# Kernel optimization log

Measured on AMD Instinct MI355X. Metric: run time of the kernel, lower is better.

## Reference

```python
import jax, jax.numpy as jnp
import numpy as np

B, S, H, NH, I = 8, 1024, 1024, 16, 4096
HD = H // NH
EPS = 1e-6
NEG = -1e9


def _glorot(key, shape):
    lim = np.sqrt(6.0 / (shape[0] + shape[1]))
    return jax.random.uniform(key, shape, jnp.float32, -lim, lim)


def setup_inputs() -> dict:
    key = jax.random.key(0)
    ks = jax.random.split(key, 8)
    return {
        "inputs": jax.random.normal(ks[0], (B, S, H), jnp.float32),
        "inputs_mask": jnp.zeros((B, S), jnp.float32),  # 1.0 marks padding
        "attn_qkvw": _glorot(ks[1], (H, 3 * H)),
        "attn_qkvb": jnp.zeros((3 * H,), jnp.float32),
        "attn_ow": _glorot(ks[2], (H, H)),
        "attn_ob": jnp.zeros((H,), jnp.float32),
        "attn_nw": jnp.ones((H,), jnp.float32),
        "attn_nb": jnp.zeros((H,), jnp.float32),
        "inter_w": _glorot(ks[3], (H, I)),
        "inter_b": jnp.zeros((I,), jnp.float32),
        "output_w": _glorot(ks[4], (I, H)),
        "output_b": jnp.zeros((H,), jnp.float32),
        "ffn_nw": jnp.ones((H,), jnp.float32),
        "ffn_nb": jnp.zeros((H,), jnp.float32),
    }


def _layer_norm(x, g, b):
    m = jnp.mean(x, axis=-1, keepdims=True)
    v = jnp.mean(jnp.square(x - m), axis=-1, keepdims=True)
    return (x - m) * jax.lax.rsqrt(v + EPS) * g + b


def reference(inputs, inputs_mask, attn_qkvw, attn_qkvb, attn_ow, attn_ob,
              attn_nw, attn_nb, inter_w, inter_b, output_w, output_b,
              ffn_nw, ffn_nb):
    # ---- self-attention block (pre-LN) ----
    res = inputs
    x = _layer_norm(inputs, attn_nw, attn_nb)
    qkv = x @ attn_qkvw + attn_qkvb                      # [B,S,3H]
    q, k, v = jnp.split(qkv, 3, axis=-1)
    q = q.reshape(B, S, NH, HD)
    k = k.reshape(B, S, NH, HD)
    v = v.reshape(B, S, NH, HD)
    scale = 1.0 / np.sqrt(HD)
    scores = jnp.einsum("bqhd,bkhd->bhqk", q, k) * scale
    scores = scores + inputs_mask[:, None, None, :] * NEG
    probs = jax.nn.softmax(scores, axis=-1)
    ctx = jnp.einsum("bhqk,bkhd->bqhd", probs, v).reshape(B, S, H)
    attn_out = ctx @ attn_ow + attn_ob
    x = res + attn_out
    # ---- FFN block (pre-LN, ReLU) ----
    res2 = x
    y = _layer_norm(x, ffn_nw, ffn_nb)
    h = jax.nn.relu(y @ inter_w + inter_b)
    return res2 + h @ output_w + output_b
```

## Files before the change

### kernel.cpp

```cpp
#include <hip/hip_runtime.h>
#include <cstdint>
#include <cstddef>

typedef _Float16 f16;
typedef _Float16 half8 __attribute__((ext_vector_type(8)));
typedef _Float16 half4v __attribute__((ext_vector_type(4)));
typedef float floatx4 __attribute__((ext_vector_type(4)));
typedef float floatx16 __attribute__((ext_vector_type(16)));

__device__ __forceinline__ floatx4 mfma16(half8 a, half8 b, floatx4 c) {
    return __builtin_amdgcn_mfma_f32_16x16x32_f16(a, b, c, 0, 0, 0);
}
__device__ __forceinline__ floatx16 mfma32(half8 a, half8 b, floatx16 c) {
    return __builtin_amdgcn_mfma_f32_32x32x16_f16(a, b, c, 0, 0, 0);
}

__device__ __forceinline__ void async16(const f16* g, f16* l) {
    __builtin_amdgcn_global_load_lds(
        (const __attribute__((address_space(1))) unsigned int*)(uintptr_t)g,
        (__attribute__((address_space(3))) unsigned int*)(uintptr_t)l,
        16, 0, 0);
}

__global__ __launch_bounds__(256)
void ln_f16_kernel(const float* __restrict__ x, const float* __restrict__ g,
                   const float* __restrict__ be, f16* __restrict__ y)
{
    int row = blockIdx.x, t = threadIdx.x;
    const float* xr = x + (size_t)row * 1024;
    float4 v = *(const float4*)(xr + t * 4);
    float s1 = v.x + v.y + v.z + v.w;
    float s2 = v.x * v.x + v.y * v.y + v.z * v.z + v.w * v.w;
    #pragma unroll
    for (int off = 32; off >= 1; off >>= 1) {
        s1 += __shfl_xor(s1, off);
        s2 += __shfl_xor(s2, off);
    }
    __shared__ float r1[4], r2[4];
    if ((t & 63) == 0) { r1[t >> 6] = s1; r2[t >> 6] = s2; }
    __syncthreads();
    s1 = r1[0] + r1[1] + r1[2] + r1[3];
    s2 = r2[0] + r2[1] + r2[2] + r2[3];
    float mean = s1 * 0.0009765625f;
    float var  = s2 * 0.0009765625f - mean * mean;
    float rs = rsqrtf(var + 1e-6f);
    float4 gv = *(const float4*)(g + t * 4);
    float4 bv = *(const float4*)(be + t * 4);
    half4v o;
    o[0] = (f16)((v.x - mean) * rs * gv.x + bv.x);
    o[1] = (f16)((v.y - mean) * rs * gv.y + bv.y);
    o[2] = (f16)((v.z - mean) * rs * gv.z + bv.z);
    o[3] = (f16)((v.w - mean) * rs * gv.w + bv.w);
    *(half4v*)(y + (size_t)row * 1024 + t * 4) = o;
}

__global__ __launch_bounds__(256)
void transpose_f16_kernel(const float* __restrict__ W, f16* __restrict__ WT,
                          int R, int C)
{
    __shared__ float tile[32][33];
    int tx = threadIdx.x & 31, ty0 = threadIdx.x >> 5;
    int r0 = blockIdx.y * 32, c0 = blockIdx.x * 32;
    #pragma unroll
    for (int i = 0; i < 4; ++i)
        tile[ty0 + i * 8][tx] = W[(size_t)(r0 + ty0 + i * 8) * C + c0 + tx];
    __syncthreads();
    #pragma unroll
    for (int i = 0; i < 4; ++i)
        WT[(size_t)(c0 + ty0 + i * 8) * R + r0 + tx] = (f16)tile[tx][ty0 + i * 8];
}

__global__ __launch_bounds__(256, 2)
void gemm_kernel(const f16* __restrict__ A, const f16* __restrict__ BT,
                 const float* __restrict__ bias, const float* __restrict__ res,
                 float* __restrict__ Cf32, int M, int N, int K)
{
    __shared__ __align__(16) f16 As[2][128 * 64];
    __shared__ __align__(16) f16 Bs[2][128 * 64];
    int m0 = blockIdx.x * 128, n0 = blockIdx.y * 128;
    int t = threadIdx.x, lane = t & 63, wave = t >> 6;
    int quad = lane >> 4, l16 = lane & 15;
    int wm = (wave & 1) * 64, wn = (wave >> 1) * 64;
    int sw = l16 & 7;
    floatx4 acc[4][4] = {};

    const f16* gA[4]; const f16* gB[4]; int oS[4];
    #pragma unroll
    for (int c = 0; c < 4; ++c) {
        int s = c * 256 + t;
        int row = s >> 3, lg = (s & 7) ^ (row & 7);
        gA[c] = A  + (size_t)(m0 + row) * K + lg * 8;
        gB[c] = BT + (size_t)(n0 + row) * K + lg * 8;
        oS[c] = (c * 256 + (t & ~63)) * 8;
    }

    #pragma unroll
    for (int c = 0; c < 4; ++c) {
        async16(gA[c], As[0] + oS[c]);
        async16(gB[c], Bs[0] + oS[c]);
    }
    __syncthreads();

    int buf = 0;
    for (int k0 = 0; k0 < K; k0 += 64) {
        int kn = k0 + 64;
        if (kn < K) {
            #pragma unroll
            for (int c = 0; c < 4; ++c) {
                async16(gA[c] + kn, As[buf ^ 1] + oS[c]);
                async16(gB[c] + kn, Bs[buf ^ 1] + oS[c]);
            }
        }
        #pragma unroll
        for (int ks = 0; ks < 2; ++ks) {
            int ca = (ks * 4 + quad) ^ sw;
            half8 a[4], b[4];
            #pragma unroll
            for (int i = 0; i < 4; ++i) {
                a[i] = *(const half8*)(As[buf] + (wm + i * 16 + l16) * 64 + ca * 8);
                b[i] = *(const half8*)(Bs[buf] + (wn + i * 16 + l16) * 64 + ca * 8);
            }
            #pragma unroll
            for (int i = 0; i < 4; ++i)
                #pragma unroll
                for (int j = 0; j < 4; ++j)
                    acc[i][j] = mfma16(a[i], b[j], acc[i][j]);
        }
        __syncthreads();
        buf ^= 1;
    }

    #pragma unroll
    for (int j = 0; j < 4; ++j) {
        int col = n0 + wn + j * 16 + l16;
        float bv = bias[col];
        #pragma unroll
        for (int i = 0; i < 4; ++i) {
            int rowb = m0 + wm + i * 16 + quad * 4;
            #pragma unroll
            for (int r = 0; r < 4; ++r) {
                float v = acc[i][j][r] + bv;
                size_t idx = (size_t)(rowb + r) * N + col;
                Cf32[idx] = v + res[idx];
            }
        }
    }
}

template<int MODE>
__global__ __launch_bounds__(256, 2)
void gemm_big_kernel(const f16* __restrict__ A, const f16* __restrict__ BT,
                     const float* __restrict__ bias, f16* __restrict__ Cf16,
                     f16* __restrict__ qb, f16* __restrict__ kb, f16* __restrict__ vb,
                     int M, int N, int K)
{
    __shared__ __align__(16) f16 As[2][256 * 32];
    __shared__ __align__(16) f16 Bs[2][128 * 32];
    int m0 = blockIdx.x * 256, n0 = blockIdx.y * 128;
    int t = threadIdx.x, lane = t & 63, wave = t >> 6;
    int l32 = lane & 31, kg = lane >> 5;
    int swz = (l32 ^ (l32 >> 2) ^ (l32 >> 4)) & 3;
    floatx16 acc[2][4];
    #pragma unroll
    for (int mi = 0; mi < 2; ++mi)
        #pragma unroll
        for (int jn = 0; jn < 4; ++jn)
            #pragma unroll
            for (int r = 0; r < 16; ++r) acc[mi][jn][r] = 0.f;

    const f16* gA[4]; int oA[4];
    #pragma unroll
    for (int c = 0; c < 4; ++c) {
        int s = c * 256 + t;
        int row = s >> 2, phys = s & 3;
        int lg = phys ^ ((row ^ (row >> 2) ^ (row >> 4)) & 3);
        gA[c] = A + (size_t)(m0 + row) * K + lg * 8;
        oA[c] = (c * 256 + (t & ~63)) * 8;
    }
    const f16* gB[2]; int oB[2];
    #pragma unroll
    for (int c = 0; c < 2; ++c) {
        int s = c * 256 + t;
        int row = s >> 2, phys = s & 3;
        int lg = phys ^ ((row ^ (row >> 2) ^ (row >> 4)) & 3);
        gB[c] = BT + (size_t)(n0 + row) * K + lg * 8;
        oB[c] = (c * 256 + (t & ~63)) * 8;
    }

    #pragma unroll
    for (int c = 0; c < 4; ++c) async16(gA[c], As[0] + oA[c]);
    #pragma unroll
    for (int c = 0; c < 2; ++c) async16(gB[c], Bs[0] + oB[c]);
    __syncthreads();

    int buf = 0;
    for (int k0 = 0; k0 < K; k0 += 32) {
        int kn = k0 + 32;
        if (kn < K) {
            #pragma unroll
            for (int c = 0; c < 4; ++c) async16(gA[c] + kn, As[buf ^ 1] + oA[c]);
            #pragma unroll
            for (int c = 0; c < 2; ++c) async16(gB[c] + kn, Bs[buf ^ 1] + oB[c]);
        }
        #pragma unroll
        for (int ss = 0; ss < 2; ++ss) {
            int cb = ss * 2 + kg;
            half8 a[2], b[4];
            #pragma unroll
            for (int mi = 0; mi < 2; ++mi) {
                int ca = (cb ^ swz ^ (mi * 2));
                a[mi] = *(const half8*)(As[buf] + (wave * 64 + mi * 32 + l32) * 32 + ca * 8);
            }
            #pragma unroll
            for (int jn = 0; jn < 4; ++jn) {
                int ca = (cb ^ swz ^ ((jn & 1) * 2));
                b[jn] = *(const half8*)(Bs[buf] + (jn * 32 + l32) * 32 + ca * 8);
            }
            #pragma unroll
            for (int mi = 0; mi < 2; ++mi)
                #pragma unroll
                for (int jn = 0; jn < 4; ++jn)
                    acc[mi][jn] = mfma32(a[mi], b[jn], acc[mi][jn]);
        }
        __syncthreads();
        buf ^= 1;
    }

    #pragma unroll
    for (int mi = 0; mi < 2; ++mi) {
        int mbase = m0 + wave * 64 + mi * 32 + 4 * kg;
        #pragma unroll
        for (int jn = 0; jn < 4; ++jn) {
            int col = n0 + jn * 32 + l32;
            float bv = bias[col];
            if (MODE == 1) {
                #pragma unroll
                for (int reg = 0; reg < 16; ++reg) {
                    int row = mbase + (reg & 3) + 8 * (reg >> 2);
                    Cf16[(size_t)row * N + col] = (f16)fmaxf(acc[mi][jn][reg] + bv, 0.f);
                }
            } else {
                int part = col >> 10;
                int h = (col >> 6) & 15;
                int d = col & 63;
                if (part == 2) {
                    #pragma unroll
                    for (int rb = 0; rb < 4; ++rb) {
                        int m = mbase + 8 * rb;
                        int bb = m >> 10, s = m & 1023;
                        size_t bh = (size_t)bb * 16 + h;
                        half4v pv;
                        #pragma unroll
                        for (int r = 0; r < 4; ++r) pv[r] = (f16)(acc[mi][jn][rb * 4 + r] + bv);
                        *(half4v*)(vb + (bh * 64 + d) * 1024 + s) = pv;
                    }
                } else {
                    f16* dst0 = part == 0 ? qb : kb;
                    #pragma unroll
                    for (int reg = 0; reg < 16; ++reg) {
                        int m = mbase + (reg & 3) + 8 * (reg >> 2);
                        int bb = m >> 10, s = m & 1023;
                        size_t bh = (size_t)bb * 16 + h;
                        dst0[(bh * 1024 + s) * 64 + d] = (f16)(acc[mi][jn][reg] + bv);
                    }
                }
            }
        }
    }
}

__global__ __launch_bounds__(256)
void attn_kernel(const f16* __restrict__ qb, const f16* __restrict__ kb,
                 const f16* __restrict__ vb, const float* __restrict__ mask,
                 f16* __restrict__ ctx)
{
    const int S = 1024;
    int qt = blockIdx.x, h = blockIdx.y, b = blockIdx.z;
    size_t bh = (size_t)b * 16 + h;
    int t = threadIdx.x, lane = t & 63, wv = t >> 6;
    int quad = lane >> 4, l16 = lane & 15;
    int sw = l16 & 7;

    __shared__ __align__(16) f16 Ks[64 * 64];
    __shared__ __align__(16) f16 Vs[64 * 64];
    __shared__ __align__(16) f16 Ps[4][16 * 40];

    int q0 = qt * 64 + wv * 16;
    const f16* qrow = qb + (bh * 1024 + q0 + l16) * 64;
    half8 aq0 = *(const half8*)(qrow + quad * 8);
    half8 aq1 = *(const half8*)(qrow + 32 + quad * 8);

    floatx4 o[4] = {};
    float lsum[4] = {0.f, 0.f, 0.f, 0.f};
    const float scale = 0.125f;
    const float* mrow = mask + b * S;

    for (int kc = 0; kc < S; kc += 64) {
        __syncthreads();
        #pragma unroll
        for (int c = 0; c < 2; ++c) {
            int s = c * 256 + t;
            int row = s >> 3, phys = s & 7;
            int lg = phys ^ (row & 7);
            f16* lk = Ks + (size_t)(c * 256 + (t & ~63)) * 8;
            f16* lv = Vs + (size_t)(c * 256 + (t & ~63)) * 8;
            async16(kb + (bh * 1024 + kc + row) * 64 + lg * 8, lk);
            async16(vb + (bh * 64 + row) * 1024 + kc + lg * 8, lv);
        }
        __syncthreads();

        floatx4 sf[4];
        #pragma unroll
        for (int cg = 0; cg < 4; ++cg) {
            const f16* kr = Ks + (cg * 16 + l16) * 64;
            int c0 = quad ^ sw;
            half8 b0 = *(const half8*)(kr + c0 * 8);
            half8 b1 = *(const half8*)(kr + (c0 ^ 4) * 8);
            floatx4 z = {};
            sf[cg] = mfma16(aq1, b1, mfma16(aq0, b0, z));
        }
        #pragma unroll
        for (int cg = 0; cg < 4; ++cg) {
            float mk = mrow[kc + cg * 16 + l16] * (-1e9f);
            #pragma unroll
            for (int r = 0; r < 4; ++r) {
                float e = __expf(sf[cg][r] * scale + mk);
                lsum[r] += e;
                Ps[wv][(quad * 4 + r) * 40 + cg * 16 + l16] = (f16)e;
            }
        }
        half8 ap0 = *(const half8*)(Ps[wv] + l16 * 40 + quad * 8);
        half8 ap1 = *(const half8*)(Ps[wv] + l16 * 40 + 32 + quad * 8);
        #pragma unroll
        for (int td = 0; td < 4; ++td) {
            const f16* vr = Vs + (td * 16 + l16) * 64;
            int c0 = quad ^ sw;
            half8 bv0 = *(const half8*)(vr + c0 * 8);
            half8 bv1 = *(const half8*)(vr + (c0 ^ 4) * 8);
            o[td] = mfma16(ap0, bv0, o[td]);
            o[td] = mfma16(ap1, bv1, o[td]);
        }
    }

    #pragma unroll
    for (int r = 0; r < 4; ++r) {
        float s = lsum[r];
        s += __shfl_xor(s, 1); s += __shfl_xor(s, 2);
        s += __shfl_xor(s, 4); s += __shfl_xor(s, 8);
        lsum[r] = 1.f / s;
    }
    #pragma unroll
    for (int td = 0; td < 4; ++td)
        #pragma unroll
        for (int r = 0; r < 4; ++r)
            ctx[((size_t)b * 1024 + q0 + quad * 4 + r) * 1024 + h * 64 + td * 16 + l16]
                = (f16)(o[td][r] * lsum[r]);
}

extern "C" void kernel_launch(void* const* d_in, const int* in_sizes, int n_in,
                              void* d_out, int out_size, void* d_ws, size_t ws_size,
                              hipStream_t stream)
{
    const float* inputs = (const float*)d_in[0];
    const float* mask   = (const float*)d_in[1];
    const float* qkvw   = (const float*)d_in[2];
    const float* qkvb   = (const float*)d_in[3];
    const float* ow     = (const float*)d_in[4];
    const float* ob     = (const float*)d_in[5];
    const float* anw    = (const float*)d_in[6];
    const float* anb    = (const float*)d_in[7];
    const float* iw     = (const float*)d_in[8];
    const float* ib     = (const float*)d_in[9];
    const float* outw   = (const float*)d_in[10];
    const float* outb   = (const float*)d_in[11];
    const float* fnw    = (const float*)d_in[12];
    const float* fnb    = (const float*)d_in[13];
    float* out = (float*)d_out;

    const int M = 8192;
    uint8_t* ws = (uint8_t*)d_ws;
    f16* wT_qkv = (f16*)(ws + 0);
    f16* wT_o   = (f16*)(ws + 6291456);
    f16* wT_i   = (f16*)(ws + 8388608);
    f16* wT_out = (f16*)(ws + 16777216);
    f16* xln    = (f16*)(ws + 25165824);
    float* x1   = (float*)(ws + 41943040);
    f16* qbuf   = (f16*)(ws + 75497472);
    f16* kbuf   = (f16*)(ws + 92274688);
    f16* vbuf   = (f16*)(ws + 109051904);
    f16* ctx    = (f16*)(ws + 125829120);
    f16* hbuf   = (f16*)(ws + 75497472);

    transpose_f16_kernel<<<dim3(96, 32),  256, 0, stream>>>(qkvw, wT_qkv, 1024, 3072);
    transpose_f16_kernel<<<dim3(32, 32),  256, 0, stream>>>(ow,   wT_o,   1024, 1024);
    transpose_f16_kernel<<<dim3(128, 32), 256, 0, stream>>>(iw,   wT_i,   1024, 4096);
    transpose_f16_kernel<<<dim3(32, 128), 256, 0, stream>>>(outw, wT_out, 4096, 1024);

    ln_f16_kernel<<<8192, 256, 0, stream>>>(inputs, anw, anb, xln);

    gemm_big_kernel<2><<<dim3(32, 24), 256, 0, stream>>>(xln, wT_qkv, qkvb,
        nullptr, qbuf, kbuf, vbuf, M, 3072, 1024);

    attn_kernel<<<dim3(16, 16, 8), 256, 0, stream>>>(qbuf, kbuf, vbuf, mask, ctx);

    gemm_kernel<<<dim3(64, 8), 256, 0, stream>>>(ctx, wT_o, ob, inputs,
        x1, M, 1024, 1024);

    ln_f16_kernel<<<8192, 256, 0, stream>>>(x1, fnw, fnb, xln);

    gemm_big_kernel<1><<<dim3(32, 32), 256, 0, stream>>>(xln, wT_i, ib,
        hbuf, nullptr, nullptr, nullptr, M, 4096, 1024);

    gemm_kernel<<<dim3(64, 8), 256, 0, stream>>>(hbuf, wT_out, outb, x1,
        out, M, 1024, 4096);
}
```

Before: 494.9 us.

## Triple-buffer big GEMM LDS staging with partial vmcnt waits and MFMA priority

Moves the big GEMM kernel from double to triple buffering of the A/B LDS tiles, prefetching two k-steps ahead. It replaces the full __syncthreads drain with s_waitcnt vmcnt(6) plus s_barrier, so one stage of async loads can stay in flight across the barrier. The MFMA block is wrapped in s_setprio to favour matrix issue. LDS use rises from 48KB to 72KB per block, which may hurt the 2-blocks-per-CU occupancy target.

```diff
diff --git a/kernel.cpp b/kernel.cpp
--- a/kernel.cpp
+++ b/kernel.cpp
@@ -147,6 +147,13 @@
     }
 }
 
+#define BSTAGE(bi, kk) do {                                                    \
+    _Pragma("unroll")                                                          \
+    for (int c = 0; c < 4; ++c) async16(gA[c] + (kk), As[bi] + oA[c]);         \
+    _Pragma("unroll")                                                          \
+    for (int c = 0; c < 2; ++c) async16(gB[c] + (kk), Bs[bi] + oB[c]);         \
+} while (0)
+
 template<int MODE>
 __global__ __launch_bounds__(256, 2)
 void gemm_big_kernel(const f16* __restrict__ A, const f16* __restrict__ BT,
@@ -154,8 +161,8 @@
                      f16* __restrict__ qb, f16* __restrict__ kb, f16* __restrict__ vb,
                      int M, int N, int K)
 {
-    __shared__ __align__(16) f16 As[2][256 * 32];
-    __shared__ __align__(16) f16 Bs[2][128 * 32];
+    __shared__ __align__(16) f16 As[3][256 * 32];
+    __shared__ __align__(16) f16 Bs[3][128 * 32];
     int m0 = blockIdx.x * 256, n0 = blockIdx.y * 128;
     int t = threadIdx.x, lane = t & 63, wave = t >> 6;
     int l32 = lane & 31, kg = lane >> 5;
@@ -187,21 +194,17 @@
         oB[c] = (c * 256 + (t & ~63)) * 8;
     }
 
-    #pragma unroll
-    for (int c = 0; c < 4; ++c) async16(gA[c], As[0] + oA[c]);
-    #pragma unroll
-    for (int c = 0; c < 2; ++c) async16(gB[c], Bs[0] + oB[c]);
-    __syncthreads();
-
-    int buf = 0;
+    BSTAGE(0, 0);
+    BSTAGE(1, 32);
+    asm volatile("s_waitcnt vmcnt(6)" ::: "memory");
+    __builtin_amdgcn_s_barrier();
+
+    int bi = 0;
+    #pragma unroll 1
     for (int k0 = 0; k0 < K; k0 += 32) {
-        int kn = k0 + 32;
-        if (kn < K) {
-            #pragma unroll
-            for (int c = 0; c < 4; ++c) async16(gA[c] + kn, As[buf ^ 1] + oA[c]);
-            #pragma unroll
-            for (int c = 0; c < 2; ++c) async16(gB[c] + kn, Bs[buf ^ 1] + oB[c]);
-        }
+        int kn = k0 + 64;
+        int bs = bi + 2; if (bs >= 3) bs -= 3;
+        if (kn < K) BSTAGE(bs, kn);
         #pragma unroll
         for (int ss = 0; ss < 2; ++ss) {
             int cb = ss * 2 + kg;
@@ -209,21 +212,25 @@
             #pragma unroll
             for (int mi = 0; mi < 2; ++mi) {
                 int ca = (cb ^ swz ^ (mi * 2));
-                a[mi] = *(const half8*)(As[buf] + (wave * 64 + mi * 32 + l32) * 32 + ca * 8);
+                a[mi] = *(const half8*)(As[bi] + (wave * 64 + mi * 32 + l32) * 32 + ca * 8);
             }
             #pragma unroll
             for (int jn = 0; jn < 4; ++jn) {
                 int ca = (cb ^ swz ^ ((jn & 1) * 2));
-                b[jn] = *(const half8*)(Bs[buf] + (jn * 32 + l32) * 32 + ca * 8);
-            }
+                b[jn] = *(const half8*)(Bs[bi] + (jn * 32 + l32) * 32 + ca * 8);
+            }
+            __builtin_amdgcn_s_setprio(1);
             #pragma unroll
             for (int mi = 0; mi < 2; ++mi)
                 #pragma unroll
                 for (int jn = 0; jn < 4; ++jn)
                     acc[mi][jn] = mfma32(a[mi], b[jn], acc[mi][jn]);
-        }
-        __syncthreads();
-        buf ^= 1;
+            __builtin_amdgcn_s_setprio(0);
+        }
+        if (kn < K) { asm volatile("s_waitcnt vmcnt(6)" ::: "memory"); }
+        else        { asm volatile("s_waitcnt vmcnt(0)" ::: "memory"); }
+        __builtin_amdgcn_s_barrier();
+        bi = bi + 1; if (bi >= 3) bi = 0;
     }
 
     #pragma unroll
@@ -268,6 +275,7 @@
         }
     }
 }
+#undef BSTAGE
 
 __global__ __launch_bounds__(256)
 void attn_kernel(const f16* __restrict__ qb, const f16* __restrict__ kb,
```

Result: faster. 478.3 us (-3.4%).

## Double-buffer K/V tiles in attention kernel to overlap loads with compute

Applied to the files above, without the earlier changes.

Adds a second LDS buffer for the K and V tiles and issues the async global-to-LDS loads for the next 64-key chunk before computing on the current one. Per-thread source pointers are hoisted out of the loop, and the two barriers per iteration become one at the end. This is meant to hide global load latency behind the MFMA and softmax work. It doubles the K/V LDS footprint, which may reduce occupancy. Correctness depends on the barrier also covering completion of the async loads.

```diff
diff --git a/kernel.cpp b/kernel.cpp
--- a/kernel.cpp
+++ b/kernel.cpp
@@ -281,8 +281,8 @@
     int quad = lane >> 4, l16 = lane & 15;
     int sw = l16 & 7;
 
-    __shared__ __align__(16) f16 Ks[64 * 64];
-    __shared__ __align__(16) f16 Vs[64 * 64];
+    __shared__ __align__(16) f16 Ks[2][64 * 64];
+    __shared__ __align__(16) f16 Vs[2][64 * 64];
     __shared__ __align__(16) f16 Ps[4][16 * 40];
 
     int q0 = qt * 64 + wv * 16;
@@ -295,24 +295,38 @@
     const float scale = 0.125f;
     const float* mrow = mask + b * S;
 
+    const f16* pK[2]; const f16* pV[2]; int oS[2];
+    #pragma unroll
+    for (int c = 0; c < 2; ++c) {
+        int s = c * 256 + t;
+        int row = s >> 3, lg = (s & 7) ^ (row & 7);
+        pK[c] = kb + (bh * 1024 + row) * 64 + lg * 8;
+        pV[c] = vb + (bh * 64 + row) * 1024 + lg * 8;
+        oS[c] = (c * 256 + (t & ~63)) * 8;
+    }
+
+    #pragma unroll
+    for (int c = 0; c < 2; ++c) {
+        async16(pK[c], Ks[0] + oS[c]);
+        async16(pV[c], Vs[0] + oS[c]);
+    }
+    __syncthreads();
+
+    int buf = 0;
     for (int kc = 0; kc < S; kc += 64) {
-        __syncthreads();
-        #pragma unroll
-        for (int c = 0; c < 2; ++c) {
-            int s = c * 256 + t;
-            int row = s >> 3, phys = s & 7;
-            int lg = phys ^ (row & 7);
-            f16* lk = Ks + (size_t)(c * 256 + (t & ~63)) * 8;
-            f16* lv = Vs + (size_t)(c * 256 + (t & ~63)) * 8;
-            async16(kb + (bh * 1024 + kc + row) * 64 + lg * 8, lk);
-            async16(vb + (bh * 64 + row) * 1024 + kc + lg * 8, lv);
-        }
-        __syncthreads();
+        int kn = kc + 64;
+        if (kn < S) {
+            #pragma unroll
+            for (int c = 0; c < 2; ++c) {
+                async16(pK[c] + (size_t)kn * 64, Ks[buf ^ 1] + oS[c]);
+                async16(pV[c] + kn,              Vs[buf ^ 1] + oS[c]);
+            }
+        }
 
         floatx4 sf[4];
         #pragma unroll
         for (int cg = 0; cg < 4; ++cg) {
-            const f16* kr = Ks + (cg * 16 + l16) * 64;
+            const f16* kr = Ks[buf] + (cg * 16 + l16) * 64;
             int c0 = quad ^ sw;
             half8 b0 = *(const half8*)(kr + c0 * 8);
             half8 b1 = *(const half8*)(kr + (c0 ^ 4) * 8);
@@ -333,13 +347,15 @@
         half8 ap1 = *(const half8*)(Ps[wv] + l16 * 40 + 32 + quad * 8);
         #pragma unroll
         for (int td = 0; td < 4; ++td) {
-            const f16* vr = Vs + (td * 16 + l16) * 64;
+            const f16* vr = Vs[buf] + (td * 16 + l16) * 64;
             int c0 = quad ^ sw;
             half8 bv0 = *(const half8*)(vr + c0 * 8);
             half8 bv1 = *(const half8*)(vr + (c0 ^ 4) * 8);
             o[td] = mfma16(ap0, bv0, o[td]);
             o[td] = mfma16(ap1, bv1, o[td]);
         }
+        __syncthreads();
+        buf ^= 1;
     }
 
     #pragma unroll
```

Measured after the change: 464.5 us. -6.1%, faster.
